# Kernel tuning notes

Hardware: AMD Instinct MI355X
Metric: run time of the kernel (lower is better)

The kernel has to match this reference:

```python
import jax, jax.numpy as jnp
import numpy as np

B, T, D = 1, 2048, 2048
NH, NKV, HD = 16, 4, 128
N_REP = NH // NKV
EPS = 1e-6
SCALE = HD ** -0.5
ROPE_THETA = 10000.0


def _rms_norm(x, w):
    # normalize over last (head_dim) axis, learned scale w[HD]
    var = jnp.mean(jnp.square(x), axis=-1, keepdims=True)
    return x * jax.lax.rsqrt(var + EPS) * w


def _rotate_half(x):
    h = x.shape[-1] // 2
    return jnp.concatenate([-x[..., h:], x[..., :h]], axis=-1)


def setup_inputs() -> dict:
    key = jax.random.key(0)
    ks = jax.random.split(key, 8)
    hidden_BTD = jax.random.normal(ks[0], (B, T, D), dtype=jnp.float32)
    # RoPE tables over full head_dim (half frequencies duplicated)
    pos = jnp.arange(T, dtype=jnp.float32)
    inv_freq = 1.0 / (ROPE_THETA ** (jnp.arange(0, HD, 2, dtype=jnp.float32) / HD))
    freqs = pos[:, None] * inv_freq[None, :]              # [T, HD/2]
    emb = jnp.concatenate([freqs, freqs], axis=-1)        # [T, HD]
    cos_BTK = jnp.broadcast_to(jnp.cos(emb)[None], (B, T, HD))
    sin_BTK = jnp.broadcast_to(jnp.sin(emb)[None], (B, T, HD))
    segment_ids_BT = jnp.sort(jax.random.randint(ks[1], (B, T), 0, 4), axis=-1).astype(jnp.int32)
    position_ids_BT = jnp.broadcast_to(jnp.arange(T, dtype=jnp.int32)[None], (B, T))
    s = 0.02
    wq = jax.random.normal(ks[2], (D, NH * HD * 2), dtype=jnp.float32) * s
    wk = jax.random.normal(ks[3], (D, NKV * HD), dtype=jnp.float32) * s
    wv = jax.random.normal(ks[4], (D, NKV * HD), dtype=jnp.float32) * s
    wo = jax.random.normal(ks[5], (NH * HD, D), dtype=jnp.float32) * s
    q_norm_w = jnp.ones((HD,), dtype=jnp.float32)
    k_norm_w = jnp.ones((HD,), dtype=jnp.float32)
    return {"hidden_BTD": hidden_BTD, "cos_BTK": cos_BTK, "sin_BTK": sin_BTK,
            "segment_ids_BT": segment_ids_BT, "position_ids_BT": position_ids_BT,
            "wq": wq, "wk": wk, "wv": wv, "wo": wo,
            "q_norm_w": q_norm_w, "k_norm_w": k_norm_w}


def reference(hidden_BTD, cos_BTK, sin_BTK, segment_ids_BT, position_ids_BT,
              wq, wk, wv, wo, q_norm_w, k_norm_w):
    Bb, Tt, _ = hidden_BTD.shape
    q_out = (hidden_BTD @ wq).reshape(Bb, Tt, NH, HD * 2)
    q_BTHK, gate_BTHK = jnp.split(q_out, 2, axis=-1)
    gate_BTD = gate_BTHK.reshape(Bb, Tt, NH * HD)
    q = _rms_norm(q_BTHK, q_norm_w).transpose(0, 2, 1, 3)                       # [B,NH,T,HD]
    k = _rms_norm((hidden_BTD @ wk).reshape(Bb, Tt, NKV, HD), k_norm_w).transpose(0, 2, 1, 3)
    v = (hidden_BTD @ wv).reshape(Bb, Tt, NKV, HD).transpose(0, 2, 1, 3)        # [B,NKV,T,HD]
    cos = cos_BTK[:, None, :, :]
    sin = sin_BTK[:, None, :, :]
    q = q * cos + _rotate_half(q) * sin
    k = k * cos + _rotate_half(k) * sin
    if N_REP > 1:
        k = jnp.repeat(k, N_REP, axis=1)
        v = jnp.repeat(v, N_REP, axis=1)
    logits = jnp.einsum('bhtk,bhsk->bhts', q, k) * SCALE                        # [B,NH,T,T]
    causal = position_ids_BT[:, None, :] <= position_ids_BT[:, :, None]         # [B,T,T]
    seg = segment_ids_BT[:, :, None] == segment_ids_BT[:, None, :]
    mask = (causal & seg)[:, None, :, :]
    neg = jnp.asarray(jnp.finfo(logits.dtype).min, logits.dtype)
    logits = jnp.where(mask, logits, neg)
    weights = jax.nn.softmax(logits.astype(jnp.float32), axis=-1).astype(logits.dtype)
    attn = jnp.einsum('bhts,bhsk->bhtk', weights, v)
    attn = attn.transpose(0, 2, 1, 3).reshape(Bb, Tt, NH * HD)
    attn = attn * jax.nn.sigmoid(gate_BTD)
    return attn @ wo
```

## Files before the change

kernel.cpp:

```cpp
#include <hip/hip_runtime.h>

typedef __attribute__((ext_vector_type(8))) short bf16x8;
typedef __attribute__((ext_vector_type(4))) float f32x4;
typedef __attribute__((ext_vector_type(4))) unsigned short us4;

#define T_SEQ 2048
#define DMODEL 2048
#define NH 16
#define NKV 4
#define HD 128
#define STRQKV 5120
#define KOFF 4096
#define VOFF 4608
#define ATT_SCALE 0.08838834764831845f
#define LOG2E 1.4426950408889634f

__device__ __forceinline__ float bf2f(unsigned short u) {
  union { unsigned int u; float f; } v; v.u = ((unsigned int)u) << 16; return v.f;
}
__device__ __forceinline__ unsigned short f2bf(float f) {
  union { float f; unsigned int u; } v; v.f = f;
  unsigned int u = v.u;
  return (unsigned short)((u + 0x7fffu + ((u >> 16) & 1u)) >> 16);
}
__device__ __forceinline__ f32x4 mfma16(bf16x8 a, bf16x8 b, f32x4 c) {
  return __builtin_amdgcn_mfma_f32_16x16x32_bf16(a, b, c, 0, 0, 0);
}
__device__ __forceinline__ void gload16(const void* g, void* l) {
  __builtin_amdgcn_global_load_lds(
      (const __attribute__((address_space(1))) unsigned int*)g,
      (__attribute__((address_space(3))) unsigned int*)l, 16, 0, 0);
}

__global__ __launch_bounds__(256) void prep(
    const float* __restrict__ hidden, const float* __restrict__ wq,
    const float* __restrict__ wk, const float* __restrict__ wv,
    const float* __restrict__ wo,
    unsigned short* __restrict__ Xb, unsigned short* __restrict__ Wqkvt,
    unsigned short* __restrict__ Wot) {
  const int bid = blockIdx.x;
  const int tid = threadIdx.x;
  if (bid < 4096) {
    int i = bid * 256 + tid;
    float4 v = ((const float4*)hidden)[i];
    us4 o; o.x = f2bf(v.x); o.y = f2bf(v.y); o.z = f2bf(v.z); o.w = f2bf(v.w);
    ((us4*)Xb)[i] = o;
    return;
  }
  const float* in; unsigned short* out; int N, lb;
  if (bid < 12288)      { in = wq; out = Wqkvt;                          N = 4096; lb = bid - 4096; }
  else if (bid < 13312) { in = wk; out = Wqkvt + (size_t)KOFF * DMODEL;  N = 512;  lb = bid - 12288; }
  else if (bid < 14336) { in = wv; out = Wqkvt + (size_t)VOFF * DMODEL;  N = 512;  lb = bid - 13312; }
  else                  { in = wo; out = Wot;                            N = 2048; lb = bid - 14336; }
  const int ntb = N >> 5;
  const int nb = (lb % ntb) * 32, kb = (lb / ntb) * 32;
  __shared__ unsigned short tile[32][33];
  const int tx = tid & 31, ty = tid >> 5;
#pragma unroll
  for (int i = 0; i < 32; i += 8)
    tile[ty + i][tx] = f2bf(in[(size_t)(kb + ty + i) * N + nb + tx]);
  __syncthreads();
#pragma unroll
  for (int i = 0; i < 32; i += 8)
    out[(size_t)(nb + ty + i) * DMODEL + kb + tx] = tile[tx][ty + i];
}

__global__ __launch_bounds__(256) void transpose_wo(
    const float* __restrict__ in, unsigned short* __restrict__ out) {
  __shared__ unsigned short tile[32][33];
  int nb = blockIdx.x * 32, kb = blockIdx.y * 32;
  int tx = threadIdx.x & 31, ty = threadIdx.x >> 5;
#pragma unroll
  for (int i = 0; i < 32; i += 8)
    tile[ty + i][tx] = f2bf(in[(size_t)(kb + ty + i) * DMODEL + nb + tx]);
  __syncthreads();
#pragma unroll
  for (int i = 0; i < 32; i += 8)
    out[(size_t)(nb + ty + i) * DMODEL + kb + tx] = tile[tx][ty + i];
}

__global__ __launch_bounds__(256) void normtv(
    unsigned short* __restrict__ qkv, unsigned short* __restrict__ vTg,
    const float* __restrict__ cosb, const float* __restrict__ sinb,
    const float* __restrict__ knw) {
  const int bid = blockIdx.x;
  const int tid = threadIdx.x;
  if (bid < 4096) {
    const int sub = tid >> 7, d = tid & 127;
    const int j = bid * 2 + sub;
    const int t = j >> 2, kh = j & 3;
    size_t addr = (size_t)t * STRQKV + KOFF + kh * HD + d;
    float x = bf2f(qkv[addr]);
    float ss = x * x;
#pragma unroll
    for (int mk = 1; mk < 64; mk <<= 1) ss += __shfl_xor(ss, mk, 64);
    __shared__ float red[4];
    __shared__ float xs[256];
    if ((tid & 63) == 0) red[tid >> 6] = ss;
    __syncthreads();
    float rstd = rsqrtf((red[sub * 2] + red[sub * 2 + 1]) * (1.0f / 128.0f) + 1e-6f);
    float xn = x * rstd * knw[d];
    xs[tid] = xn;
    __syncthreads();
    float other = (d < 64) ? -xs[sub * 128 + d + 64] : xs[sub * 128 + d - 64];
    qkv[addr] = f2bf(xn * cosb[(size_t)t * HD + d] + other * sinb[(size_t)t * HD + d]);
    return;
  }
  const int lb = bid - 4096;
  const int tb = (lb & 63) * 32, db = ((lb >> 6) & 3) * 32, kvh = lb >> 8;
  __shared__ unsigned short tile[32][33];
  const int tx = tid & 31, ty = tid >> 5;
#pragma unroll
  for (int i = 0; i < 32; i += 8)
    tile[ty + i][tx] = qkv[(size_t)(tb + ty + i) * STRQKV + VOFF + kvh * HD + db + tx];
  __syncthreads();
#pragma unroll
  for (int i = 0; i < 32; i += 8)
    vTg[((size_t)kvh * HD + db + ty + i) * T_SEQ + tb + tx] = tile[tx][ty + i];
}

template <typename OT>
__global__ __launch_bounds__(512) void gemm_bt(const unsigned short* __restrict__ A,
                                               const unsigned short* __restrict__ B,
                                               OT* __restrict__ C, int M, int N, int K) {
  __shared__ unsigned short As[2][128 * 32];
  __shared__ unsigned short Bs[2][128 * 32];
  const int tid = threadIdx.x;
  const int wave = tid >> 6, lane = tid & 63;
  const int wr = wave >> 1, wc = wave & 1;
  const int g = lane >> 4, lr = lane & 15;
  const int row0 = blockIdx.y * 128, col0 = blockIdx.x * 128;

  const unsigned short* Ap = A + (size_t)(row0 + (tid >> 2)) * K + (tid & 3) * 8;
  const unsigned short* Bp = B + (size_t)(col0 + (tid >> 2)) * K + (tid & 3) * 8;

  f32x4 acc[2][4] = {};

  auto stage = [&](int buf, int k0) {
    gload16(Ap + k0, &As[buf][tid * 8]);
    gload16(Bp + k0, &Bs[buf][tid * 8]);
  };

  stage(0, 0);
  __syncthreads();
  int cur = 0;
  for (int k0 = 0; k0 < K; k0 += 32) {
    if (k0 + 32 < K) stage(cur ^ 1, k0 + 32);

    bf16x8 af[2], bfr[4];
#pragma unroll
    for (int m = 0; m < 2; ++m) af[m] = *(const bf16x8*)(&As[cur][(wr * 32 + m * 16 + lr) * 32 + g * 8]);
#pragma unroll
    for (int n = 0; n < 4; ++n) bfr[n] = *(const bf16x8*)(&Bs[cur][(wc * 64 + n * 16 + lr) * 32 + g * 8]);
    __builtin_amdgcn_s_setprio(1);
#pragma unroll
    for (int m = 0; m < 2; ++m)
#pragma unroll
      for (int n = 0; n < 4; ++n)
        acc[m][n] = mfma16(af[m], bfr[n], acc[m][n]);
    __builtin_amdgcn_s_setprio(0);

    __syncthreads();
    cur ^= 1;
  }

#pragma unroll
  for (int m = 0; m < 2; ++m)
#pragma unroll
    for (int n = 0; n < 4; ++n)
#pragma unroll
      for (int r = 0; r < 4; ++r) {
        int row = row0 + wr * 32 + m * 16 + g * 4 + r;
        int col = col0 + wc * 64 + n * 16 + lr;
        float v = acc[m][n][r];
        if constexpr (sizeof(OT) == 2) C[(size_t)row * N + col] = f2bf(v);
        else                            C[(size_t)row * N + col] = v;
      }
}

__global__ __launch_bounds__(512) void attn_kernel(
    const unsigned short* __restrict__ qkv, const unsigned short* __restrict__ vTg,
    const int* __restrict__ seg,
    const float* __restrict__ cosb, const float* __restrict__ sinb,
    const float* __restrict__ qnw,
    unsigned short* __restrict__ attnb) {
  const int bid = blockIdx.x;
  const int h = bid & 15;
  const int j = bid >> 4;
  const int qb = (j < 8) ? j : 23 - j;
  const int kvh = h >> 2;
  const int tid = threadIdx.x;
  const int wave = tid >> 6, lane = tid & 63;
  const int g = lane >> 4, lr = lane & 15;
  const int qrow0 = qb * 128 + wave * 16;

  __shared__ unsigned short Ks[4][32 * 128];
  __shared__ unsigned short Vt[4][128 * 32];
  __shared__ unsigned short Plds[8][16][40];

  const unsigned short* Kbase = qkv + KOFF + kvh * HD;
  const unsigned short* Vbase = vTg + (size_t)kvh * HD * T_SEQ;

  auto stage = [&](int buf, int kv0) {
    {
      int row = tid >> 4;
      int c16 = (tid & 15) ^ (row & 7);
      gload16(Kbase + (size_t)(kv0 + row) * STRQKV + c16 * 8, &Ks[buf][tid * 8]);
    }
    {
      int row = tid >> 2;
      int c16 = (tid & 3) ^ (row & 3);
      gload16(Vbase + (size_t)row * T_SEQ + kv0 + c16 * 8, &Vt[buf][tid * 8]);
    }
  };

  const int ntiles = qb * 4 + 4;
  const int segB = seg[qb * 128];
  int t_begin = 0;
  while (t_begin < ntiles - 1 && seg[t_begin * 32 + 31] < segB) ++t_begin;

  stage(t_begin & 3, t_begin * 32);
  if (t_begin + 1 < ntiles) stage((t_begin + 1) & 3, t_begin * 32 + 32);

  const int t0 = qrow0 + lr;
  float xn[4][8];
  {
    float ssl = 0.f;
#pragma unroll
    for (int c = 0; c < 4; ++c) {
      bf16x8 tq = *(const bf16x8*)(qkv + (size_t)t0 * STRQKV + h * 256 + c * 32 + g * 8);
#pragma unroll
      for (int i = 0; i < 8; ++i) {
        float x = bf2f((unsigned short)tq[i]);
        xn[c][i] = x;
        ssl += x * x;
      }
    }
    ssl += __shfl_xor(ssl, 16, 64);
    ssl += __shfl_xor(ssl, 32, 64);
    float rstd = rsqrtf(ssl * (1.0f / 128.0f) + 1e-6f);
#pragma unroll
    for (int c = 0; c < 4; ++c)
#pragma unroll
      for (int i = 0; i < 8; ++i)
        xn[c][i] *= rstd * qnw[c * 32 + g * 8 + i];
  }
  bf16x8 qf[4];
#pragma unroll
  for (int c = 0; c < 4; ++c)
#pragma unroll
    for (int i = 0; i < 8; ++i) {
      int d = c * 32 + g * 8 + i;
      float rot = (c < 2) ? -xn[c + 2][i] : xn[c - 2][i];
      float ov = xn[c][i] * cosb[(size_t)t0 * HD + d] + rot * sinb[(size_t)t0 * HD + d];
      qf[c][i] = (short)f2bf(ov * (ATT_SCALE * LOG2E));
    }

  bf16x8 vones;
#pragma unroll
  for (int i = 0; i < 8; ++i) vones[i] = (short)0x3F80;

  int myrow[4], myseg[4];
#pragma unroll
  for (int r = 0; r < 4; ++r) {
    myrow[r] = qrow0 + g * 4 + r;
    myseg[r] = seg[myrow[r]];
  }
  const int seg_lo = seg[qrow0];
  const int seg_hi = seg[qrow0 + 15];

  f32x4 lacc = {};
  f32x4 oacc[8] = {};

  for (int t = t_begin; t < ntiles; ++t) {
    const int kv0 = t * 32;
    if (t + 2 < ntiles) {
      stage((t + 2) & 3, kv0 + 64);
      asm volatile("s_waitcnt vmcnt(4)" ::: "memory");
    } else if (t + 1 < ntiles) {
      asm volatile("s_waitcnt vmcnt(2)" ::: "memory");
    } else {
      asm volatile("s_waitcnt vmcnt(0)" ::: "memory");
    }
    __builtin_amdgcn_s_barrier();
    __builtin_amdgcn_sched_barrier(0);

    if (kv0 < qrow0 + 16 && seg[kv0 + 31] >= seg_lo) {
      const unsigned short* ks = Ks[t & 3];
      const unsigned short* vt = Vt[t & 3];

      f32x4 sacc[2] = {};
      __builtin_amdgcn_s_setprio(1);
#pragma unroll
      for (int cc = 0; cc < 2; ++cc)
#pragma unroll
        for (int c = 0; c < 4; ++c) {
          int row = cc * 16 + lr;
          bf16x8 kf = *(const bf16x8*)(&ks[row * 128 + (((c * 4 + g) ^ (row & 7)) * 8)]);
          sacc[cc] = mfma16(qf[c], kf, sacc[cc]);
        }
      __builtin_amdgcn_s_setprio(0);

      const bool full = (kv0 + 32 <= qrow0) && (seg[kv0] == seg_hi);
      if (full) {
#pragma unroll
        for (int cc = 0; cc < 2; ++cc)
#pragma unroll
          for (int r = 0; r < 4; ++r)
            Plds[wave][g * 4 + r][cc * 16 + lr] = f2bf(exp2f(sacc[cc][r]));
      } else {
#pragma unroll
        for (int cc = 0; cc < 2; ++cc) {
          int kvi = kv0 + cc * 16 + lr;
          int ksg = seg[kvi];
#pragma unroll
          for (int r = 0; r < 4; ++r) {
            bool ok = (kvi <= myrow[r]) && (ksg == myseg[r]);
            float p = exp2f(sacc[cc][r]);
            Plds[wave][g * 4 + r][cc * 16 + lr] = f2bf(ok ? p : 0.0f);
          }
        }
      }

      bf16x8 pf = *(const bf16x8*)(&Plds[wave][lr][g * 8]);
      __builtin_amdgcn_s_setprio(1);
#pragma unroll
      for (int n = 0; n < 8; ++n) {
        bf16x8 vf = *(const bf16x8*)(&vt[(n * 16 + lr) * 32 + ((g ^ (lr & 3)) * 8)]);
        oacc[n] = mfma16(pf, vf, oacc[n]);
      }
      lacc = mfma16(pf, vones, lacc);
      __builtin_amdgcn_s_setprio(0);
    }
  }

#pragma unroll
  for (int n = 0; n < 8; ++n)
#pragma unroll
    for (int r = 0; r < 4; ++r) {
      int row = myrow[r];
      int d = n * 16 + lr;
      float o = oacc[n][r] / lacc[r];
      float gv = bf2f(qkv[(size_t)row * STRQKV + h * 256 + 128 + d]);
      float gate = 1.0f / (1.0f + __expf(-gv));
      attnb[(size_t)row * (NH * HD) + h * HD + d] = f2bf(o * gate);
    }
}

extern "C" void kernel_launch(void* const* d_in, const int* in_sizes, int n_in,
                              void* d_out, int out_size, void* d_ws, size_t ws_size,
                              hipStream_t stream) {
  const float* hidden = (const float*)d_in[0];
  const float* cosb   = (const float*)d_in[1];
  const float* sinb   = (const float*)d_in[2];
  const int*   seg    = (const int*)d_in[3];
  const float* wq     = (const float*)d_in[5];
  const float* wk     = (const float*)d_in[6];
  const float* wv     = (const float*)d_in[7];
  const float* wo     = (const float*)d_in[8];
  const float* qnw    = (const float*)d_in[9];
  const float* knw    = (const float*)d_in[10];
  float* out = (float*)d_out;

  char* ws = (char*)d_ws;
  const size_t MB = (size_t)1 << 20;
  const bool big = ws_size >= 56 * MB;
  unsigned short* Xb    = (unsigned short*)(ws + 0 * MB);
  unsigned short* Attnb = (unsigned short*)(ws + 0 * MB);
  unsigned short* Wqkvt = (unsigned short*)(ws + 8 * MB);
  unsigned short* VT    = (unsigned short*)(ws + 16 * MB);
  unsigned short* Cqkv  = (unsigned short*)(ws + 28 * MB);
  unsigned short* Wot   = (unsigned short*)(big ? (ws + 48 * MB) : (ws + 8 * MB));

  prep<<<big ? 18432 : 14336, 256, 0, stream>>>(hidden, wq, wk, wv, wo, Xb, Wqkvt, Wot);

  gemm_bt<unsigned short><<<dim3(STRQKV / 128, T_SEQ / 128), 512, 0, stream>>>(Xb, Wqkvt, Cqkv, T_SEQ, STRQKV, DMODEL);

  if (!big)
    transpose_wo<<<dim3(DMODEL / 32, DMODEL / 32), 256, 0, stream>>>(wo, Wot);

  normtv<<<5120, 256, 0, stream>>>(Cqkv, VT, cosb, sinb, knw);

  attn_kernel<<<256, 512, 0, stream>>>(Cqkv, VT, seg, cosb, sinb, qnw, Attnb);

  gemm_bt<float><<<dim3(DMODEL / 128, T_SEQ / 128), 512, 0, stream>>>(Attnb, Wot, out, T_SEQ, DMODEL, DMODEL);
}
```

Before: 157.9 us.

## Widen QKV GEMM tile to 160 columns and use 64-key attention tiles

The QKV projection GEMM gets a templated column tile width, set to 160 so its grid is 32x16 = 512 blocks instead of 40x16 = 640, which lines up more evenly with the CU count. The attention kernel now works on 64-key K/V tiles with plain double buffering and __syncthreads, replacing 32-key tiles with a 4-deep asynchronous ring. The P tile layout in LDS is XOR-swizzled to avoid bank conflicts. Larger tiles halve the loop iterations and barriers but raise LDS use and register pressure, drop the two-tile prefetch depth, and add masking waste at the causal and segment boundaries.

```diff
diff --git a/kernel.cpp b/kernel.cpp
--- a/kernel.cpp
+++ b/kernel.cpp
@@ -119,26 +119,31 @@
     vTg[((size_t)kvh * HD + db + ty + i) * T_SEQ + tb + tx] = tile[tx][ty + i];
 }
 
-template <typename OT>
+template <int BN, typename OT>
 __global__ __launch_bounds__(512) void gemm_bt(const unsigned short* __restrict__ A,
                                                const unsigned short* __restrict__ B,
                                                OT* __restrict__ C, int M, int N, int K) {
+  constexpr int NB = BN / 32;
   __shared__ unsigned short As[2][128 * 32];
-  __shared__ unsigned short Bs[2][128 * 32];
+  __shared__ unsigned short Bs[2][BN * 32];
   const int tid = threadIdx.x;
   const int wave = tid >> 6, lane = tid & 63;
   const int wr = wave >> 1, wc = wave & 1;
   const int g = lane >> 4, lr = lane & 15;
-  const int row0 = blockIdx.y * 128, col0 = blockIdx.x * 128;
-
-  const unsigned short* Ap = A + (size_t)(row0 + (tid >> 2)) * K + (tid & 3) * 8;
-  const unsigned short* Bp = B + (size_t)(col0 + (tid >> 2)) * K + (tid & 3) * 8;
-
-  f32x4 acc[2][4] = {};
+  const int row0 = blockIdx.y * 128, col0 = blockIdx.x * BN;
+
+  const unsigned short* Ap  = A + (size_t)(row0 + (tid >> 2)) * K + (tid & 3) * 8;
+  const unsigned short* Bp  = B + (size_t)(col0 + (tid >> 2)) * K + (tid & 3) * 8;
+  const unsigned short* Bp2 = B + (size_t)(col0 + 128 + (tid >> 2)) * K + (tid & 3) * 8;
+
+  f32x4 acc[2][NB] = {};
 
   auto stage = [&](int buf, int k0) {
     gload16(Ap + k0, &As[buf][tid * 8]);
     gload16(Bp + k0, &Bs[buf][tid * 8]);
+    if constexpr (BN == 160) {
+      if (tid < 128) gload16(Bp2 + k0, &Bs[buf][4096 + tid * 8]);
+    }
   };
 
   stage(0, 0);
@@ -147,16 +152,16 @@
   for (int k0 = 0; k0 < K; k0 += 32) {
     if (k0 + 32 < K) stage(cur ^ 1, k0 + 32);
 
-    bf16x8 af[2], bfr[4];
+    bf16x8 af[2], bfr[NB];
 #pragma unroll
     for (int m = 0; m < 2; ++m) af[m] = *(const bf16x8*)(&As[cur][(wr * 32 + m * 16 + lr) * 32 + g * 8]);
 #pragma unroll
-    for (int n = 0; n < 4; ++n) bfr[n] = *(const bf16x8*)(&Bs[cur][(wc * 64 + n * 16 + lr) * 32 + g * 8]);
+    for (int n = 0; n < NB; ++n) bfr[n] = *(const bf16x8*)(&Bs[cur][(wc * (BN / 2) + n * 16 + lr) * 32 + g * 8]);
     __builtin_amdgcn_s_setprio(1);
 #pragma unroll
     for (int m = 0; m < 2; ++m)
 #pragma unroll
-      for (int n = 0; n < 4; ++n)
+      for (int n = 0; n < NB; ++n)
         acc[m][n] = mfma16(af[m], bfr[n], acc[m][n]);
     __builtin_amdgcn_s_setprio(0);
 
@@ -167,11 +172,11 @@
 #pragma unroll
   for (int m = 0; m < 2; ++m)
 #pragma unroll
-    for (int n = 0; n < 4; ++n)
+    for (int n = 0; n < NB; ++n)
 #pragma unroll
       for (int r = 0; r < 4; ++r) {
         int row = row0 + wr * 32 + m * 16 + g * 4 + r;
-        int col = col0 + wc * 64 + n * 16 + lr;
+        int col = col0 + wc * (BN / 2) + n * 16 + lr;
         float v = acc[m][n][r];
         if constexpr (sizeof(OT) == 2) C[(size_t)row * N + col] = f2bf(v);
         else                            C[(size_t)row * N + col] = v;
@@ -194,33 +199,34 @@
   const int g = lane >> 4, lr = lane & 15;
   const int qrow0 = qb * 128 + wave * 16;
 
-  __shared__ unsigned short Ks[4][32 * 128];
-  __shared__ unsigned short Vt[4][128 * 32];
-  __shared__ unsigned short Plds[8][16][40];
+  __shared__ unsigned short Ks[2][64 * 128];
+  __shared__ unsigned short Vt[2][128 * 64];
+  __shared__ unsigned short Plds[8][16][64];
 
   const unsigned short* Kbase = qkv + KOFF + kvh * HD;
   const unsigned short* Vbase = vTg + (size_t)kvh * HD * T_SEQ;
 
   auto stage = [&](int buf, int kv0) {
-    {
-      int row = tid >> 4;
+#pragma unroll
+    for (int i = 0; i < 2; ++i) {
+      int row = i * 32 + (tid >> 4);
       int c16 = (tid & 15) ^ (row & 7);
-      gload16(Kbase + (size_t)(kv0 + row) * STRQKV + c16 * 8, &Ks[buf][tid * 8]);
-    }
-    {
-      int row = tid >> 2;
-      int c16 = (tid & 3) ^ (row & 3);
-      gload16(Vbase + (size_t)row * T_SEQ + kv0 + c16 * 8, &Vt[buf][tid * 8]);
+      gload16(Kbase + (size_t)(kv0 + row) * STRQKV + c16 * 8, &Ks[buf][i * 4096 + tid * 8]);
+    }
+#pragma unroll
+    for (int i = 0; i < 2; ++i) {
+      int row = i * 64 + (tid >> 3);
+      int c16 = (tid & 7) ^ (row & 7);
+      gload16(Vbase + (size_t)row * T_SEQ + kv0 + c16 * 8, &Vt[buf][i * 4096 + tid * 8]);
     }
   };
 
-  const int ntiles = qb * 4 + 4;
+  const int ntiles = qb * 2 + 2;
   const int segB = seg[qb * 128];
   int t_begin = 0;
-  while (t_begin < ntiles - 1 && seg[t_begin * 32 + 31] < segB) ++t_begin;
-
-  stage(t_begin & 3, t_begin * 32);
-  if (t_begin + 1 < ntiles) stage((t_begin + 1) & 3, t_begin * 32 + 32);
+  while (t_begin < ntiles - 1 && seg[t_begin * 64 + 63] < segB) ++t_begin;
+
+  stage(0, t_begin * 64);
 
   const int t0 = qrow0 + lr;
   float xn[4][8];
@@ -272,27 +278,20 @@
   f32x4 lacc = {};
   f32x4 oacc[8] = {};
 
+  __syncthreads();
+  int cur = 0;
   for (int t = t_begin; t < ntiles; ++t) {
-    const int kv0 = t * 32;
-    if (t + 2 < ntiles) {
-      stage((t + 2) & 3, kv0 + 64);
-      asm volatile("s_waitcnt vmcnt(4)" ::: "memory");
-    } else if (t + 1 < ntiles) {
-      asm volatile("s_waitcnt vmcnt(2)" ::: "memory");
-    } else {
-      asm volatile("s_waitcnt vmcnt(0)" ::: "memory");
-    }
-    __builtin_amdgcn_s_barrier();
-    __builtin_amdgcn_sched_barrier(0);
-
-    if (kv0 < qrow0 + 16 && seg[kv0 + 31] >= seg_lo) {
-      const unsigned short* ks = Ks[t & 3];
-      const unsigned short* vt = Vt[t & 3];
-
-      f32x4 sacc[2] = {};
+    const int kv0 = t * 64;
+    if (t + 1 < ntiles) stage(cur ^ 1, kv0 + 64);
+
+    if (kv0 < qrow0 + 16 && seg[kv0 + 63] >= seg_lo) {
+      const unsigned short* ks = Ks[cur];
+      const unsigned short* vt = Vt[cur];
+
+      f32x4 sacc[4] = {};
       __builtin_amdgcn_s_setprio(1);
 #pragma unroll
-      for (int cc = 0; cc < 2; ++cc)
+      for (int cc = 0; cc < 4; ++cc)
 #pragma unroll
         for (int c = 0; c < 4; ++c) {
           int row = cc * 16 + lr;
@@ -301,37 +300,45 @@
         }
       __builtin_amdgcn_s_setprio(0);
 
-      const bool full = (kv0 + 32 <= qrow0) && (seg[kv0] == seg_hi);
+      const bool full = (kv0 + 64 <= qrow0) && (seg[kv0] == seg_hi);
       if (full) {
 #pragma unroll
-        for (int cc = 0; cc < 2; ++cc)
+        for (int cc = 0; cc < 4; ++cc)
 #pragma unroll
           for (int r = 0; r < 4; ++r)
-            Plds[wave][g * 4 + r][cc * 16 + lr] = f2bf(exp2f(sacc[cc][r]));
+            Plds[wave][g * 4 + r][((cc ^ r) * 16) + lr] = f2bf(exp2f(sacc[cc][r]));
       } else {
 #pragma unroll
-        for (int cc = 0; cc < 2; ++cc) {
+        for (int cc = 0; cc < 4; ++cc) {
           int kvi = kv0 + cc * 16 + lr;
           int ksg = seg[kvi];
 #pragma unroll
           for (int r = 0; r < 4; ++r) {
             bool ok = (kvi <= myrow[r]) && (ksg == myseg[r]);
             float p = exp2f(sacc[cc][r]);
-            Plds[wave][g * 4 + r][cc * 16 + lr] = f2bf(ok ? p : 0.0f);
+            Plds[wave][g * 4 + r][((cc ^ r) * 16) + lr] = f2bf(ok ? p : 0.0f);
           }
         }
       }
 
-      bf16x8 pf = *(const bf16x8*)(&Plds[wave][lr][g * 8]);
+      bf16x8 pf0 = *(const bf16x8*)(&Plds[wave][lr][(g * 8) ^ ((lr & 3) << 4)]);
+      bf16x8 pf1 = *(const bf16x8*)(&Plds[wave][lr][(32 + g * 8) ^ ((lr & 3) << 4)]);
       __builtin_amdgcn_s_setprio(1);
 #pragma unroll
       for (int n = 0; n < 8; ++n) {
-        bf16x8 vf = *(const bf16x8*)(&vt[(n * 16 + lr) * 32 + ((g ^ (lr & 3)) * 8)]);
-        oacc[n] = mfma16(pf, vf, oacc[n]);
+        int row = n * 16 + lr;
+        bf16x8 vf0 = *(const bf16x8*)(&vt[row * 64 + ((g ^ (row & 7)) * 8)]);
+        oacc[n] = mfma16(pf0, vf0, oacc[n]);
+        bf16x8 vf1 = *(const bf16x8*)(&vt[row * 64 + (((4 + g) ^ (row & 7)) * 8)]);
+        oacc[n] = mfma16(pf1, vf1, oacc[n]);
       }
-      lacc = mfma16(pf, vones, lacc);
+      lacc = mfma16(pf0, vones, lacc);
+      lacc = mfma16(pf1, vones, lacc);
       __builtin_amdgcn_s_setprio(0);
     }
+
+    __syncthreads();
+    cur ^= 1;
   }
 
 #pragma unroll
@@ -374,7 +381,7 @@
 
   prep<<<big ? 18432 : 14336, 256, 0, stream>>>(hidden, wq, wk, wv, wo, Xb, Wqkvt, Wot);
 
-  gemm_bt<unsigned short><<<dim3(STRQKV / 128, T_SEQ / 128), 512, 0, stream>>>(Xb, Wqkvt, Cqkv, T_SEQ, STRQKV, DMODEL);
+  gemm_bt<160, unsigned short><<<dim3(STRQKV / 160, T_SEQ / 128), 512, 0, stream>>>(Xb, Wqkvt, Cqkv, T_SEQ, STRQKV, DMODEL);
 
   if (!big)
     transpose_wo<<<dim3(DMODEL / 32, DMODEL / 32), 256, 0, stream>>>(wo, Wot);
@@ -383,5 +390,5 @@
 
   attn_kernel<<<256, 512, 0, stream>>>(Cqkv, VT, seg, cosb, sinb, qnw, Attnb);
 
-  gemm_bt<float><<<dim3(DMODEL / 128, T_SEQ / 128), 512, 0, stream>>>(Attnb, Wot, out, T_SEQ, DMODEL, DMODEL);
-}
+  gemm_bt<128, float><<<dim3(DMODEL / 128, T_SEQ / 128), 512, 0, stream>>>(Attnb, Wot, out, T_SEQ, DMODEL, DMODEL);
+}
```

Measured after the change: 150.1 us. 1.05x faster.
